# Performance work log

Hardware: AMD Instinct MI355X
Metric: run time of the kernel (lower is better)

Reference implementation:

```python
import jax, jax.numpy as jnp
import numpy as np

N, D, K = 10240, 256, 30  # nodes, feature dim, top-k
EPS = 1e-12  # F.normalize eps


def setup_inputs() -> dict:
    key = jax.random.key(0)
    k1, _ = jax.random.split(key)
    features = jax.random.normal(k1, (N, D), dtype=jnp.float32)
    # Attentive layers: elementwise feature weights, initialized to ones (as in the repo)
    w1 = jnp.ones((D,), dtype=jnp.float32)
    w2 = jnp.ones((D,), dtype=jnp.float32)
    return {"features": features, "w1": w1, "w2": w2, "k": K}


def reference(features, w1, w2, k):
    # internal_forward: Attentive = x * w (x @ diag(w)); relu between layers (mlp_act='relu')
    h = jax.nn.relu(features * w1) * w2              # [N, D]
    # F.normalize(dim=1, p=2) with eps clamp
    norm = jnp.maximum(jnp.linalg.norm(h, axis=1, keepdims=True), EPS)
    emb = h / norm                                   # [N, D]
    # cal_similarity_graph: dense cosine similarity
    sim = emb @ emb.T                                # [N, N]
    # top_k(sim, k+1): keep top (k+1) entries per row, zero the rest
    _, idx = jax.lax.top_k(sim, k + 1)               # [N, k+1]
    rows = jnp.arange(sim.shape[0])[:, None]
    mask = jnp.zeros_like(sim).at[rows, idx].set(1.0)
    # apply_non_linearity with 'relu'
    return jax.nn.relu(sim * mask)
```

## Files before the change

### kernel.cpp

```cpp
#include <hip/hip_runtime.h>
#include <math.h>

#define N_NODES 10240
#define DIM 256
#define TPB 256
#define CAP 1536

typedef _Float16 half8 __attribute__((ext_vector_type(8)));
typedef float f32x4 __attribute__((ext_vector_type(4)));

__device__ __forceinline__ void async_load16(const void* g, void* l) {
  __builtin_amdgcn_global_load_lds(
      (const __attribute__((address_space(1))) unsigned int*)g,
      (__attribute__((address_space(3))) unsigned int*)l, 16, 0, 0);
}

__global__ __launch_bounds__(256) void norm_split_kernel(
    const float* __restrict__ F, const float* __restrict__ w1,
    const float* __restrict__ w2, _Float16* __restrict__ P0,
    _Float16* __restrict__ P1) {
  int row = blockIdx.x, tid = threadIdx.x;
  __shared__ float red[TPB];
  size_t base = (size_t)row * DIM + tid;
  float h = fmaxf(F[base] * w1[tid], 0.0f) * w2[tid];
  red[tid] = h * h;
  __syncthreads();
  for (int o = TPB / 2; o > 0; o >>= 1) {
    if (tid < o) red[tid] += red[tid + o];
    __syncthreads();
  }
  float e = h / fmaxf(sqrtf(red[0]), 1e-12f);
  _Float16 p0 = (_Float16)e;
  _Float16 p1 = (_Float16)((e - (float)p0) * 2048.0f);
  P0[base] = p0;
  P1[base] = p1;
}

__global__ __launch_bounds__(256) void gemm_mfma_kernel(
    const _Float16* __restrict__ P0, const _Float16* __restrict__ P1,
    float* __restrict__ C) {
  __shared__ char smem[32768];
  char* AsB = smem;
  char* BsB = smem + 16384;

  int tid = threadIdx.x;
  int lane = tid & 63;
  int w = tid >> 6;
  int wr = (w >> 1) * 64;
  int wc = (w & 1) * 64;
  int quad = lane >> 4;
  int mr = lane & 15;
  int rowBase = blockIdx.y * 128;
  int colBase = blockIdx.x * 128;

  size_t rowOffA[4], rowOffB[4];
  int ldsOff[4];
#pragma unroll
  for (int i = 0; i < 4; ++i) {
    int u = tid + i * 256;
    int m = u >> 3;
    int g = (u & 7) ^ (m & 7);
    ldsOff[i] = u * 16;
    rowOffA[i] = (size_t)(rowBase + m) * DIM + g * 8;
    rowOffB[i] = (size_t)(colBase + m) * DIM + g * 8;
  }

  int fOffA[2][4], fOffB[2][4];
#pragma unroll
  for (int s = 0; s < 2; ++s)
#pragma unroll
    for (int t = 0; t < 4; ++t) {
      int g = s * 4 + quad;
      int mA = wr + t * 16 + mr;
      fOffA[s][t] = (mA * 8 + (g ^ (mA & 7))) * 16;
      int mB = wc + t * 16 + mr;
      fOffB[s][t] = (mB * 8 + (g ^ (mB & 7))) * 16;
    }

  f32x4 acc[4][4];
#pragma unroll
  for (int t = 0; t < 4; ++t)
#pragma unroll
    for (int u2 = 0; u2 < 4; ++u2) acc[t][u2] = (f32x4)0.0f;

  const _Float16* Aseg[3] = {P0, P1, P0};
  const _Float16* Bseg[3] = {P1, P0, P0};

  for (int pass = 0; pass < 3; ++pass) {
    if (pass == 2) {
      const float sc = 1.0f / 2048.0f;
#pragma unroll
      for (int t = 0; t < 4; ++t)
#pragma unroll
        for (int u2 = 0; u2 < 4; ++u2)
#pragma unroll
          for (int r = 0; r < 4; ++r) acc[t][u2][r] *= sc;
    }
    const _Float16* Ap = Aseg[pass];
    const _Float16* Bp = Bseg[pass];
    for (int c = 0; c < 4; ++c) {
      int kb = c * 64;
#pragma unroll
      for (int i = 0; i < 4; ++i)
        async_load16(Ap + rowOffA[i] + kb, AsB + ldsOff[i]);
#pragma unroll
      for (int i = 0; i < 4; ++i)
        async_load16(Bp + rowOffB[i] + kb, BsB + ldsOff[i]);
      __syncthreads();
#pragma unroll
      for (int s = 0; s < 2; ++s) {
        half8 af[4], bf[4];
#pragma unroll
        for (int t = 0; t < 4; ++t) {
          af[t] = *(const half8*)(AsB + fOffA[s][t]);
          bf[t] = *(const half8*)(BsB + fOffB[s][t]);
        }
#pragma unroll
        for (int t = 0; t < 4; ++t)
#pragma unroll
          for (int u2 = 0; u2 < 4; ++u2)
            acc[t][u2] = __builtin_amdgcn_mfma_f32_16x16x32_f16(
                af[t], bf[u2], acc[t][u2], 0, 0, 0);
      }
      __syncthreads();
    }
  }

#pragma unroll
  for (int t = 0; t < 4; ++t) {
    int gr = rowBase + wr + t * 16 + quad * 4;
#pragma unroll
    for (int u2 = 0; u2 < 4; ++u2) {
      int gc = colBase + wc + u2 * 16 + mr;
      float* cp = C + (size_t)gr * N_NODES + gc;
      cp[0] = acc[t][u2][0];
      cp[(size_t)N_NODES] = acc[t][u2][1];
      cp[(size_t)2 * N_NODES] = acc[t][u2][2];
      cp[(size_t)3 * N_NODES] = acc[t][u2][3];
    }
  }
}

__global__ __launch_bounds__(256) void topk_kernel(
    float* __restrict__ C, const int* __restrict__ kptr) {
  constexpr int EPT = N_NODES / TPB;
  constexpr int NV4 = EPT / 4;
  __shared__ unsigned int lm[TPB];
  __shared__ unsigned int cu[CAP];
  __shared__ int ci[CAP];
  __shared__ unsigned int s_cnt, s_L31, s_Tu;
  __shared__ int s_Jcut;

  int tid = threadIdx.x;
  float* Crow = C + (size_t)blockIdx.x * N_NODES;
  unsigned int want = (unsigned int)(kptr[0] + 1);

  unsigned int u[EPT];
  unsigned int lmax = 0u;
#pragma unroll
  for (int i = 0; i < NV4; ++i) {
    float4 v = *(const float4*)&Crow[(i * TPB + tid) * 4];
    float fv[4] = {v.x, v.y, v.z, v.w};
#pragma unroll
    for (int c = 0; c < 4; ++c) {
      unsigned int s = __float_as_uint(fv[c]);
      unsigned int m = (s & 0x80000000u) ? ~s : (s | 0x80000000u);
      u[i * 4 + c] = m;
      lmax = (m > lmax) ? m : lmax;
    }
  }
  lm[tid] = lmax;
  if (tid == 0) s_cnt = 0u;
  __syncthreads();

  {
    unsigned int r = 0;
    for (int j = 0; j < TPB; ++j) {
      unsigned int vj = lm[j];
      r += (vj > lmax) || (vj == lmax && j < tid);
    }
    if (r == want - 1) s_L31 = lmax;
  }
  __syncthreads();
  unsigned int L31 = s_L31;

#pragma unroll
  for (int i = 0; i < EPT; ++i) {
    if (u[i] >= L31) {
      unsigned int pos = atomicAdd(&s_cnt, 1u);
      if (pos < CAP) {
        cu[pos] = u[i];
        ci[pos] = ((i / 4) * TPB + tid) * 4 + (i % 4);
      }
    }
  }
  __syncthreads();
  unsigned int c_total = s_cnt;

  if (c_total <= CAP) {
    for (unsigned int i = tid; i < c_total; i += TPB) {
      unsigned int ui = cu[i];
      int ii = ci[i];
      unsigned int r = 0;
      for (unsigned int j = 0; j < c_total; ++j) {
        unsigned int uj = cu[j];
        r += (uj > ui) || (uj == ui && ci[j] < ii);
      }
      if (r == want - 1) { s_Tu = ui; s_Jcut = ii; }
    }
    __syncthreads();
  } else {
    unsigned int lo = 0u, hi = 0xFFFFFFFFu;
    while (lo < hi) {
      unsigned int mid = lo + ((hi - lo) >> 1);
      unsigned int cnt = 0;
#pragma unroll
      for (int i = 0; i < EPT; ++i) cnt += (u[i] > mid) ? 1u : 0u;
      lm[tid] = cnt;
      __syncthreads();
      for (int o = TPB / 2; o > 0; o >>= 1) {
        if (tid < o) lm[tid] += lm[tid + o];
        __syncthreads();
      }
      unsigned int gcnt = lm[0];
      __syncthreads();
      if (gcnt < want) hi = mid; else lo = mid + 1u;
    }
    unsigned int Tu = lo;
    unsigned int cnt = 0;
#pragma unroll
    for (int i = 0; i < EPT; ++i) cnt += (u[i] > Tu) ? 1u : 0u;
    lm[tid] = cnt;
    __syncthreads();
    for (int o = TPB / 2; o > 0; o >>= 1) {
      if (tid < o) lm[tid] += lm[tid + o];
      __syncthreads();
    }
    unsigned int need = want - lm[0];
    __syncthreads();
    int jlo = 0, jhi = N_NODES - 1;
    while (jlo < jhi) {
      int jmid = (jlo + jhi) >> 1;
      unsigned int cc = 0;
#pragma unroll
      for (int i = 0; i < EPT; ++i) {
        int jj = ((i / 4) * TPB + tid) * 4 + (i % 4);
        cc += (u[i] == Tu && jj <= jmid) ? 1u : 0u;
      }
      lm[tid] = cc;
      __syncthreads();
      for (int o = TPB / 2; o > 0; o >>= 1) {
        if (tid < o) lm[tid] += lm[tid + o];
        __syncthreads();
      }
      unsigned int tot = lm[0];
      __syncthreads();
      if (tot >= need) jhi = jmid; else jlo = jmid + 1;
    }
    if (tid == 0) { s_Tu = Tu; s_Jcut = jlo; }
    __syncthreads();
  }

  unsigned int Tu = s_Tu;
  int Jcut = s_Jcut;

#pragma unroll
  for (int i = 0; i < NV4; ++i) {
    float out[4];
#pragma unroll
    for (int c = 0; c < 4; ++c) {
      unsigned int m = u[i * 4 + c];
      int j = (i * TPB + tid) * 4 + c;
      bool keep = (m > Tu) || (m == Tu && j <= Jcut);
      float v = __uint_as_float((m & 0x80000000u) ? (m ^ 0x80000000u) : ~m);
      out[c] = (keep && v > 0.0f) ? v : 0.0f;
    }
    *(float4*)&Crow[(i * TPB + tid) * 4] =
        make_float4(out[0], out[1], out[2], out[3]);
  }
}

extern "C" void kernel_launch(void* const* d_in, const int* in_sizes, int n_in,
                              void* d_out, int out_size, void* d_ws, size_t ws_size,
                              hipStream_t stream) {
  const float* F  = (const float*)d_in[0];
  const float* w1 = (const float*)d_in[1];
  const float* w2 = (const float*)d_in[2];
  const int*   kp = (const int*)d_in[3];
  float* C = (float*)d_out;
  _Float16* P0 = (_Float16*)d_ws;
  _Float16* P1 = P0 + (size_t)N_NODES * DIM;

  norm_split_kernel<<<N_NODES, DIM, 0, stream>>>(F, w1, w2, P0, P1);

  dim3 grid(N_NODES / 128, N_NODES / 128);
  gemm_mfma_kernel<<<grid, 256, 0, stream>>>(P0, P1, C);

  topk_kernel<<<N_NODES, TPB, 0, stream>>>(C, kp);
}
```

Measured before the change: 666.8 us.

## Fuse three split-precision GEMM passes into one K-loop with dual accumulators

The three sequential passes over K, each reloading a P0/P1 tile pair, become a single K-loop. That loop stages all four tiles (A0, A1, B0, B1) in 64KB of LDS and accumulates the main product and the cross terms in separate register sets, combining them with the 1/2048 scale at the end. This cuts global/LDS loads and barrier count per output tile by reusing the loaded tiles across the three products. In exchange it doubles accumulator registers and LDS use, which may lower occupancy.

```diff
diff --git a/kernel.cpp b/kernel.cpp
--- a/kernel.cpp
+++ b/kernel.cpp
@@ -39,9 +39,11 @@
 __global__ __launch_bounds__(256) void gemm_mfma_kernel(
     const _Float16* __restrict__ P0, const _Float16* __restrict__ P1,
     float* __restrict__ C) {
-  __shared__ char smem[32768];
-  char* AsB = smem;
-  char* BsB = smem + 16384;
+  __shared__ char smem[65536];
+  char* A0 = smem;
+  char* A1 = smem + 16384;
+  char* B0 = smem + 32768;
+  char* B1 = smem + 49152;
 
   int tid = threadIdx.x;
   int lane = tid & 63;
@@ -77,66 +79,86 @@
       fOffB[s][t] = (mB * 8 + (g ^ (mB & 7))) * 16;
     }
 
-  f32x4 acc[4][4];
+  f32x4 accM[4][4], accX[4][4];
 #pragma unroll
   for (int t = 0; t < 4; ++t)
 #pragma unroll
-    for (int u2 = 0; u2 < 4; ++u2) acc[t][u2] = (f32x4)0.0f;
-
-  const _Float16* Aseg[3] = {P0, P1, P0};
-  const _Float16* Bseg[3] = {P1, P0, P0};
-
-  for (int pass = 0; pass < 3; ++pass) {
-    if (pass == 2) {
-      const float sc = 1.0f / 2048.0f;
+    for (int u2 = 0; u2 < 4; ++u2) {
+      accM[t][u2] = (f32x4)0.0f;
+      accX[t][u2] = (f32x4)0.0f;
+    }
+
+  for (int c = 0; c < 4; ++c) {
+    int kb = c * 64;
+#pragma unroll
+    for (int i = 0; i < 4; ++i)
+      async_load16(P0 + rowOffA[i] + kb, A0 + ldsOff[i]);
+#pragma unroll
+    for (int i = 0; i < 4; ++i)
+      async_load16(P1 + rowOffA[i] + kb, A1 + ldsOff[i]);
+#pragma unroll
+    for (int i = 0; i < 4; ++i)
+      async_load16(P0 + rowOffB[i] + kb, B0 + ldsOff[i]);
+#pragma unroll
+    for (int i = 0; i < 4; ++i)
+      async_load16(P1 + rowOffB[i] + kb, B1 + ldsOff[i]);
+    __syncthreads();
+
+#pragma unroll
+    for (int s = 0; s < 2; ++s) {
+      half8 a0[4], b0[4];
+#pragma unroll
+      for (int t = 0; t < 4; ++t) {
+        a0[t] = *(const half8*)(A0 + fOffA[s][t]);
+        b0[t] = *(const half8*)(B0 + fOffB[s][t]);
+      }
 #pragma unroll
       for (int t = 0; t < 4; ++t)
 #pragma unroll
         for (int u2 = 0; u2 < 4; ++u2)
-#pragma unroll
-          for (int r = 0; r < 4; ++r) acc[t][u2][r] *= sc;
-    }
-    const _Float16* Ap = Aseg[pass];
-    const _Float16* Bp = Bseg[pass];
-    for (int c = 0; c < 4; ++c) {
-      int kb = c * 64;
-#pragma unroll
-      for (int i = 0; i < 4; ++i)
-        async_load16(Ap + rowOffA[i] + kb, AsB + ldsOff[i]);
-#pragma unroll
-      for (int i = 0; i < 4; ++i)
-        async_load16(Bp + rowOffB[i] + kb, BsB + ldsOff[i]);
-      __syncthreads();
-#pragma unroll
-      for (int s = 0; s < 2; ++s) {
-        half8 af[4], bf[4];
-#pragma unroll
-        for (int t = 0; t < 4; ++t) {
-          af[t] = *(const half8*)(AsB + fOffA[s][t]);
-          bf[t] = *(const half8*)(BsB + fOffB[s][t]);
-        }
-#pragma unroll
-        for (int t = 0; t < 4; ++t)
-#pragma unroll
-          for (int u2 = 0; u2 < 4; ++u2)
-            acc[t][u2] = __builtin_amdgcn_mfma_f32_16x16x32_f16(
-                af[t], bf[u2], acc[t][u2], 0, 0, 0);
-      }
-      __syncthreads();
-    }
-  }
-
+          accM[t][u2] = __builtin_amdgcn_mfma_f32_16x16x32_f16(
+              a0[t], b0[u2], accM[t][u2], 0, 0, 0);
+
+      half8 a1[4];
+#pragma unroll
+      for (int t = 0; t < 4; ++t)
+        a1[t] = *(const half8*)(A1 + fOffA[s][t]);
+#pragma unroll
+      for (int t = 0; t < 4; ++t)
+#pragma unroll
+        for (int u2 = 0; u2 < 4; ++u2)
+          accX[t][u2] = __builtin_amdgcn_mfma_f32_16x16x32_f16(
+              a1[t], b0[u2], accX[t][u2], 0, 0, 0);
+
+      half8 b1[4];
+#pragma unroll
+      for (int t = 0; t < 4; ++t)
+        b1[t] = *(const half8*)(B1 + fOffB[s][t]);
+#pragma unroll
+      for (int t = 0; t < 4; ++t)
+#pragma unroll
+        for (int u2 = 0; u2 < 4; ++u2)
+          accX[t][u2] = __builtin_amdgcn_mfma_f32_16x16x32_f16(
+              a0[t], b1[u2], accX[t][u2], 0, 0, 0);
+    }
+    __syncthreads();
+  }
+
+  const float sc = 1.0f / 2048.0f;
 #pragma unroll
   for (int t = 0; t < 4; ++t) {
     int gr = rowBase + wr + t * 16 + quad * 4;
 #pragma unroll
     for (int u2 = 0; u2 < 4; ++u2) {
       int gc = colBase + wc + u2 * 16 + mr;
+      f32x4 v;
+#pragma unroll
+      for (int r = 0; r < 4; ++r) v[r] = accM[t][u2][r] + accX[t][u2][r] * sc;
       float* cp = C + (size_t)gr * N_NODES + gc;
-      cp[0] = acc[t][u2][0];
-      cp[(size_t)N_NODES] = acc[t][u2][1];
-      cp[(size_t)2 * N_NODES] = acc[t][u2][2];
-      cp[(size_t)3 * N_NODES] = acc[t][u2][3];
+      cp[0] = v[0];
+      cp[(size_t)N_NODES] = v[1];
+      cp[(size_t)2 * N_NODES] = v[2];
+      cp[(size_t)3 * N_NODES] = v[3];
     }
   }
 }
```

Result: slower. 748.6 us (+12.3%).

## Emit per-tile row maxima from GEMM to prune top-k candidate scan

Applied to the files above, without the earlier changes.

The GEMM epilogue now computes, for each row, the maximum over each 128-column tile and writes it to a small workspace array. The top-k kernel uses these tile maxima to find a lower bound L, then reads only the tiles whose maximum is at least L instead of the whole row. The final pass writes zeros everywhere except the selected columns, which it looks up through a bitmap. This cuts most of the read traffic on the similarity matrix in top-k, at the cost of extra shuffles and atomics in the GEMM epilogue. It also drops the fallback path for candidate overflow, so candidates beyond CAP are silently truncated.

```diff
diff --git a/kernel.cpp b/kernel.cpp
--- a/kernel.cpp
+++ b/kernel.cpp
@@ -4,7 +4,9 @@
 #define N_NODES 10240
 #define DIM 256
 #define TPB 256
-#define CAP 1536
+#define NBLK (N_NODES / 128)
+#define CAP 1024
+#define KMAX 96
 
 typedef _Float16 half8 __attribute__((ext_vector_type(8)));
 typedef float f32x4 __attribute__((ext_vector_type(4)));
@@ -13,6 +15,14 @@
   __builtin_amdgcn_global_load_lds(
       (const __attribute__((address_space(1))) unsigned int*)g,
       (__attribute__((address_space(3))) unsigned int*)l, 16, 0, 0);
+}
+
+__device__ __forceinline__ unsigned int fmap(float f) {
+  unsigned int s = __float_as_uint(f);
+  return (s & 0x80000000u) ? ~s : (s | 0x80000000u);
+}
+__device__ __forceinline__ float funmap(unsigned int m) {
+  return __uint_as_float((m & 0x80000000u) ? (m ^ 0x80000000u) : ~m);
 }
 
 __global__ __launch_bounds__(256) void norm_split_kernel(
@@ -38,7 +48,7 @@
 
 __global__ __launch_bounds__(256) void gemm_mfma_kernel(
     const _Float16* __restrict__ P0, const _Float16* __restrict__ P1,
-    float* __restrict__ C) {
+    float* __restrict__ C, unsigned int* __restrict__ Dg) {
   __shared__ char smem[32768];
   char* AsB = smem;
   char* BsB = smem + 16384;
@@ -126,6 +136,25 @@
     }
   }
 
+  unsigned int* dls = (unsigned int*)smem;
+  if (tid < 128) dls[tid] = 0u;
+  __syncthreads();
+#pragma unroll
+  for (int t = 0; t < 4; ++t) {
+#pragma unroll
+    for (int r = 0; r < 4; ++r) {
+      float v = fmaxf(fmaxf(acc[t][0][r], acc[t][1][r]),
+                      fmaxf(acc[t][2][r], acc[t][3][r]));
+#pragma unroll
+      for (int mlane = 1; mlane < 16; mlane <<= 1)
+        v = fmaxf(v, __shfl_xor(v, mlane, 64));
+      if (mr == 0) atomicMax(&dls[wr + t * 16 + quad * 4 + r], fmap(v));
+    }
+  }
+  __syncthreads();
+  if (tid < 128)
+    Dg[(size_t)(rowBase + tid) * NBLK + blockIdx.x] = dls[tid];
+
 #pragma unroll
   for (int t = 0; t < 4; ++t) {
     int gr = rowBase + wr + t * 16 + quad * 4;
@@ -142,141 +171,106 @@
 }
 
 __global__ __launch_bounds__(256) void topk_kernel(
-    float* __restrict__ C, const int* __restrict__ kptr) {
-  constexpr int EPT = N_NODES / TPB;
-  constexpr int NV4 = EPT / 4;
-  __shared__ unsigned int lm[TPB];
+    float* __restrict__ C, const unsigned int* __restrict__ Dg,
+    const int* __restrict__ kptr) {
+  __shared__ unsigned int dmap[NBLK];
+  __shared__ int tlist[NBLK];
   __shared__ unsigned int cu[CAP];
   __shared__ int ci[CAP];
-  __shared__ unsigned int s_cnt, s_L31, s_Tu;
+  __shared__ unsigned int bitmap[N_NODES / 32];
+  __shared__ float kv[KMAX];
+  __shared__ int kc[KMAX];
+  __shared__ unsigned int s_nt, s_cnt, s_nk, s_L, s_Tu;
   __shared__ int s_Jcut;
 
   int tid = threadIdx.x;
-  float* Crow = C + (size_t)blockIdx.x * N_NODES;
+  int row = blockIdx.x;
+  float* Crow = C + (size_t)row * N_NODES;
   unsigned int want = (unsigned int)(kptr[0] + 1);
 
-  unsigned int u[EPT];
-  unsigned int lmax = 0u;
-#pragma unroll
-  for (int i = 0; i < NV4; ++i) {
-    float4 v = *(const float4*)&Crow[(i * TPB + tid) * 4];
-    float fv[4] = {v.x, v.y, v.z, v.w};
-#pragma unroll
-    for (int c = 0; c < 4; ++c) {
-      unsigned int s = __float_as_uint(fv[c]);
-      unsigned int m = (s & 0x80000000u) ? ~s : (s | 0x80000000u);
-      u[i * 4 + c] = m;
-      lmax = (m > lmax) ? m : lmax;
-    }
-  }
-  lm[tid] = lmax;
-  if (tid == 0) s_cnt = 0u;
-  __syncthreads();
-
-  {
+  if (tid < NBLK) dmap[tid] = Dg[(size_t)row * NBLK + tid];
+  if (tid == 0) { s_nt = 0u; s_cnt = 0u; s_nk = 0u; }
+  for (int b = tid; b < N_NODES / 32; b += TPB) bitmap[b] = 0u;
+  __syncthreads();
+
+  if (tid < NBLK) {
+    unsigned int v = dmap[tid];
     unsigned int r = 0;
-    for (int j = 0; j < TPB; ++j) {
-      unsigned int vj = lm[j];
-      r += (vj > lmax) || (vj == lmax && j < tid);
-    }
-    if (r == want - 1) s_L31 = lmax;
-  }
-  __syncthreads();
-  unsigned int L31 = s_L31;
-
-#pragma unroll
-  for (int i = 0; i < EPT; ++i) {
-    if (u[i] >= L31) {
-      unsigned int pos = atomicAdd(&s_cnt, 1u);
-      if (pos < CAP) {
-        cu[pos] = u[i];
-        ci[pos] = ((i / 4) * TPB + tid) * 4 + (i % 4);
-      }
-    }
-  }
-  __syncthreads();
-  unsigned int c_total = s_cnt;
-
-  if (c_total <= CAP) {
-    for (unsigned int i = tid; i < c_total; i += TPB) {
-      unsigned int ui = cu[i];
-      int ii = ci[i];
-      unsigned int r = 0;
-      for (unsigned int j = 0; j < c_total; ++j) {
-        unsigned int uj = cu[j];
-        r += (uj > ui) || (uj == ui && ci[j] < ii);
-      }
-      if (r == want - 1) { s_Tu = ui; s_Jcut = ii; }
-    }
-    __syncthreads();
-  } else {
-    unsigned int lo = 0u, hi = 0xFFFFFFFFu;
-    while (lo < hi) {
-      unsigned int mid = lo + ((hi - lo) >> 1);
-      unsigned int cnt = 0;
-#pragma unroll
-      for (int i = 0; i < EPT; ++i) cnt += (u[i] > mid) ? 1u : 0u;
-      lm[tid] = cnt;
-      __syncthreads();
-      for (int o = TPB / 2; o > 0; o >>= 1) {
-        if (tid < o) lm[tid] += lm[tid + o];
-        __syncthreads();
-      }
-      unsigned int gcnt = lm[0];
-      __syncthreads();
-      if (gcnt < want) hi = mid; else lo = mid + 1u;
-    }
-    unsigned int Tu = lo;
-    unsigned int cnt = 0;
-#pragma unroll
-    for (int i = 0; i < EPT; ++i) cnt += (u[i] > Tu) ? 1u : 0u;
-    lm[tid] = cnt;
-    __syncthreads();
-    for (int o = TPB / 2; o > 0; o >>= 1) {
-      if (tid < o) lm[tid] += lm[tid + o];
-      __syncthreads();
-    }
-    unsigned int need = want - lm[0];
-    __syncthreads();
-    int jlo = 0, jhi = N_NODES - 1;
-    while (jlo < jhi) {
-      int jmid = (jlo + jhi) >> 1;
-      unsigned int cc = 0;
-#pragma unroll
-      for (int i = 0; i < EPT; ++i) {
-        int jj = ((i / 4) * TPB + tid) * 4 + (i % 4);
-        cc += (u[i] == Tu && jj <= jmid) ? 1u : 0u;
-      }
-      lm[tid] = cc;
-      __syncthreads();
-      for (int o = TPB / 2; o > 0; o >>= 1) {
-        if (tid < o) lm[tid] += lm[tid + o];
-        __syncthreads();
-      }
-      unsigned int tot = lm[0];
-      __syncthreads();
-      if (tot >= need) jhi = jmid; else jlo = jmid + 1;
-    }
-    if (tid == 0) { s_Tu = Tu; s_Jcut = jlo; }
-    __syncthreads();
-  }
-
+    for (int j = 0; j < NBLK; ++j) {
+      unsigned int vj = dmap[j];
+      r += (vj > v) || (vj == v && j < tid);
+    }
+    if (r == want - 1) s_L = v;
+  }
+  __syncthreads();
+  unsigned int L = s_L;
+
+  if (tid < NBLK && dmap[tid] >= L) tlist[atomicAdd(&s_nt, 1u)] = tid;
+  __syncthreads();
+  int nt = (int)s_nt;
+
+  for (int tb = 0; tb < nt; tb += 2) {
+    int which = tb + (tid >> 7);
+    if (which < nt) {
+      int col = tlist[which] * 128 + (tid & 127);
+      unsigned int m = fmap(Crow[col]);
+      if (m >= L) {
+        unsigned int pos = atomicAdd(&s_cnt, 1u);
+        if (pos < CAP) { cu[pos] = m; ci[pos] = col; }
+      }
+    }
+  }
+  __syncthreads();
+  unsigned int cnt = s_cnt;
+  if (cnt > CAP) cnt = CAP;
+
+  for (unsigned int i = tid; i < cnt; i += TPB) {
+    unsigned int ui = cu[i];
+    int ii = ci[i];
+    unsigned int r = 0;
+    for (unsigned int j = 0; j < cnt; ++j) {
+      unsigned int uj = cu[j];
+      r += (uj > ui) || (uj == ui && ci[j] < ii);
+    }
+    if (r == want - 1) { s_Tu = ui; s_Jcut = ii; }
+  }
+  __syncthreads();
   unsigned int Tu = s_Tu;
   int Jcut = s_Jcut;
 
-#pragma unroll
-  for (int i = 0; i < NV4; ++i) {
-    float out[4];
-#pragma unroll
-    for (int c = 0; c < 4; ++c) {
-      unsigned int m = u[i * 4 + c];
-      int j = (i * TPB + tid) * 4 + c;
-      bool keep = (m > Tu) || (m == Tu && j <= Jcut);
-      float v = __uint_as_float((m & 0x80000000u) ? (m ^ 0x80000000u) : ~m);
-      out[c] = (keep && v > 0.0f) ? v : 0.0f;
-    }
-    *(float4*)&Crow[(i * TPB + tid) * 4] =
-        make_float4(out[0], out[1], out[2], out[3]);
+  for (unsigned int i = tid; i < cnt; i += TPB) {
+    unsigned int m = cu[i];
+    int col = ci[i];
+    if ((m > Tu) || (m == Tu && col <= Jcut)) {
+      unsigned int p = atomicAdd(&s_nk, 1u);
+      if (p < KMAX) {
+        kv[p] = fmaxf(funmap(m), 0.0f);
+        kc[p] = col;
+        atomicOr(&bitmap[col >> 5], 1u << (col & 31));
+      }
+    }
+  }
+  __syncthreads();
+  int nk = (int)s_nk;
+  if (nk > KMAX) nk = KMAX;
+
+#pragma unroll
+  for (int i = 0; i < N_NODES / (TPB * 4); ++i) {
+    int j4 = (i * TPB + tid) * 4;
+    unsigned int bits = (bitmap[j4 >> 5] >> (j4 & 31)) & 0xFu;
+    float4 o = make_float4(0.0f, 0.0f, 0.0f, 0.0f);
+    if (bits) {
+      float* oc = (float*)&o;
+#pragma unroll
+      for (int c = 0; c < 4; ++c) {
+        if ((bits >> c) & 1u) {
+          int col = j4 + c;
+          for (int s = 0; s < nk; ++s)
+            if (kc[s] == col) { oc[c] = kv[s]; break; }
+        }
+      }
+    }
+    *(float4*)&Crow[j4] = o;
   }
 }
 
@@ -290,11 +284,12 @@
   float* C = (float*)d_out;
   _Float16* P0 = (_Float16*)d_ws;
   _Float16* P1 = P0 + (size_t)N_NODES * DIM;
+  unsigned int* Dg = (unsigned int*)(P1 + (size_t)N_NODES * DIM);
 
   norm_split_kernel<<<N_NODES, DIM, 0, stream>>>(F, w1, w2, P0, P1);
 
   dim3 grid(N_NODES / 128, N_NODES / 128);
-  gemm_mfma_kernel<<<grid, 256, 0, stream>>>(P0, P1, C);
-
-  topk_kernel<<<N_NODES, TPB, 0, stream>>>(C, kp);
-}
+  gemm_mfma_kernel<<<grid, 256, 0, stream>>>(P0, P1, C, Dg);
+
+  topk_kernel<<<N_NODES, TPB, 0, stream>>>(C, Dg, kp);
+}
```

After: 761.1 us. +14.1%, slower.
